# Kernel optimization log

Hardware: AMD Instinct MI355X
Metric: run time of the kernel (lower is better)

Reference implementation:

```python
import jax, jax.numpy as jnp
import numpy as np

B, T, C, H = 4, 2048, 1024, 16
D = C // H  # head dim = 64


def setup_inputs() -> dict:
    key = jax.random.key(0)
    ks = jax.random.split(key, 5)
    s = 1.0 / np.sqrt(C)
    return {
        "x": jax.random.normal(ks[0], (B, T, C), jnp.float32),
        "Wq": jax.random.normal(ks[1], (C, C), jnp.float32) * s,
        "bq": jnp.zeros((C,), jnp.float32),
        "Wk": jax.random.normal(ks[2], (C, C), jnp.float32) * s,
        "bk": jnp.zeros((C,), jnp.float32),
        "Wv": jax.random.normal(ks[3], (C, C), jnp.float32) * s,
        "bv": jnp.zeros((C,), jnp.float32),
        "Wp": jax.random.normal(ks[4], (C, C), jnp.float32) * s,
        "bp": jnp.zeros((C,), jnp.float32),
    }


def reference(x, Wq, bq, Wk, bk, Wv, bv, Wp, bp):
    # linear projections -> [B, H, T, D]
    def heads(t):
        return t.reshape(B, T, H, D).transpose(0, 2, 1, 3)
    q = heads(x @ Wq.T + bq)
    k = heads(x @ Wk.T + bk)
    v = heads(x @ Wv.T + bv)
    scale = 1.0 / np.sqrt(D)
    att = jnp.einsum("bhtd,bhsd->bhts", q, k) * scale  # [B,H,T,T]
    causal = jnp.tril(jnp.ones((T, T), bool))
    att = jnp.where(causal[None, None], att, -jnp.inf)
    att = jax.nn.softmax(att, axis=-1)
    y = jnp.einsum("bhts,bhsd->bhtd", att, v)  # [B,H,T,D]
    y = y.transpose(0, 2, 1, 3).reshape(B, T, C)
    return y @ Wp.T + bp
```

## Files before the change

### kernel.cpp

```cpp
#include <hip/hip_runtime.h>

typedef float f32x4 __attribute__((ext_vector_type(4)));
typedef float f32x16 __attribute__((ext_vector_type(16)));
typedef __bf16 bf16x8 __attribute__((ext_vector_type(8)));
typedef unsigned short u16x8 __attribute__((ext_vector_type(8)));
typedef unsigned int u32x4 __attribute__((ext_vector_type(4)));

#define SCQ 0.1803368801111183f

__device__ inline unsigned short f2bf(float f) {
  unsigned int u = __builtin_bit_cast(unsigned int, f);
  u += 0x7FFFu + ((u >> 16) & 1u);
  return (unsigned short)(u >> 16);
}

__device__ inline float fexp2(float x) {
#if __has_builtin(__builtin_amdgcn_exp2f)
  return __builtin_amdgcn_exp2f(x);
#else
  return exp2f(x);
#endif
}

__device__ inline unsigned int cvtpk_bf16(float a, float b) {
  unsigned int r;
  __asm__("v_cvt_pk_bf16_f32 %0, %1, %2" : "=v"(r) : "v"(a), "v"(b));
  return r;
}
__device__ inline void permswap32(unsigned int& a, unsigned int& b) {
  __asm__("v_permlane32_swap_b32 %0, %1" : "+v"(a), "+v"(b));
}

__device__ inline void gload_lds16(const unsigned short* g, unsigned short* l) {
  __builtin_amdgcn_global_load_lds(
      (const __attribute__((address_space(1))) unsigned int*)g,
      (__attribute__((address_space(3))) unsigned int*)l, 16, 0, 0);
}

__global__ void cvt_x(const float* __restrict__ in, unsigned short* __restrict__ out) {
  int i = (blockIdx.x * 256 + threadIdx.x) * 4;
  float4 f = *(const float4*)(in + i);
  ushort4 o;
  o.x = f2bf(f.x); o.y = f2bf(f.y); o.z = f2bf(f.z); o.w = f2bf(f.w);
  *(ushort4*)(out + i) = o;
}

__global__ void cvt_w(const float* __restrict__ a, const float* __restrict__ b,
                      const float* __restrict__ c, const float* __restrict__ d,
                      unsigned short* __restrict__ oa, unsigned short* __restrict__ ob,
                      unsigned short* __restrict__ oc, unsigned short* __restrict__ od) {
  const float* src[4] = {a, b, c, d};
  unsigned short* dst[4] = {oa, ob, oc, od};
  int m = blockIdx.y;
  int i = (blockIdx.x * 256 + threadIdx.x) * 4;
  float4 f = *(const float4*)(src[m] + i);
  ushort4 o;
  o.x = f2bf(f.x); o.y = f2bf(f.y); o.z = f2bf(f.z); o.w = f2bf(f.w);
  *(ushort4*)(dst[m] + i) = o;
}

template <int MODE>
__global__ __launch_bounds__(512, 2) void gemm8p(const unsigned short* __restrict__ A,
                                                 const unsigned short* __restrict__ Bt,
                                                 const float* __restrict__ b0,
                                                 const float* __restrict__ b1,
                                                 const float* __restrict__ b2,
                                                 void* __restrict__ out,
                                                 int M, int N, int K) {
  __shared__ __align__(16) unsigned short Lg[2][3][128 * 64];
  const int tid = threadIdx.x;
  const int lane = tid & 63, w = tid >> 6;
  const int qm = w >> 2, qn = w & 3;
  const int l15 = lane & 15, kq = lane >> 4;
  const int m0 = blockIdx.x * 128, n0 = blockIdx.y * 256;
  const int NT = K >> 6;

  const int row0 = tid >> 3, c0 = (tid & 7) ^ (row0 & 7);
  const int row1 = row0 + 64, c1 = (tid & 7) ^ (row1 & 7);

  auto stage = [&](int tt, int h) {
    if (tt < NT) {
      const unsigned short* s_ = (h == 0) ? A : Bt;
      const int rbase = (h == 0) ? m0 : (h == 1 ? n0 : n0 + 128);
      unsigned short* d = &Lg[tt & 1][h][0];
      gload_lds16(s_ + (size_t)(rbase + row0) * K + tt * 64 + c0 * 8, d + (size_t)tid * 8);
      gload_lds16(s_ + (size_t)(rbase + row1) * K + tt * 64 + c1 * 8, d + (size_t)(tid + 512) * 8);
    }
  };

  auto rdA = [&](const unsigned short* R, u16x8 (&a)[4][2]) {
#pragma unroll
    for (int mf = 0; mf < 4; mf++) {
      int row = qm * 64 + mf * 16 + l15;
#pragma unroll
      for (int kf = 0; kf < 2; kf++) {
        int pc = (kf * 4 + kq) ^ (row & 7);
        a[mf][kf] = *(const u16x8*)(R + row * 64 + pc * 8);
      }
    }
  };
  auto rdB = [&](const unsigned short* R, u16x8 (&bb)[2][2]) {
#pragma unroll
    for (int nf = 0; nf < 2; nf++) {
      int row = qn * 32 + nf * 16 + l15;
#pragma unroll
      for (int kf = 0; kf < 2; kf++) {
        int pc = (kf * 4 + kq) ^ (row & 7);
        bb[nf][kf] = *(const u16x8*)(R + row * 64 + pc * 8);
      }
    }
  };

  f32x4 acc[4][4] = {};

  auto domfma = [&](u16x8 (&a)[4][2], u16x8 (&bb)[2][2], int hb) {
#pragma unroll
    for (int mf = 0; mf < 4; mf++)
#pragma unroll
      for (int nf = 0; nf < 2; nf++)
#pragma unroll
        for (int kf = 0; kf < 2; kf++)
          acc[mf][hb * 2 + nf] = __builtin_amdgcn_mfma_f32_16x16x32_bf16(
              __builtin_bit_cast(bf16x8, a[mf][kf]),
              __builtin_bit_cast(bf16x8, bb[nf][kf]), acc[mf][hb * 2 + nf], 0, 0, 0);
  };

  stage(0, 0); stage(0, 1); stage(0, 2); stage(1, 0); stage(1, 1);
  __asm__ __volatile__("s_waitcnt vmcnt(4)" ::: "memory");
  __builtin_amdgcn_s_barrier();

  for (int tt = 0; tt < NT; ++tt) {
    const unsigned short* Ar  = &Lg[tt & 1][0][0];
    const unsigned short* B0r = &Lg[tt & 1][1][0];
    const unsigned short* B1r = &Lg[tt & 1][2][0];
    u16x8 aA[4][2], bb[2][2];

    rdA(Ar, aA); rdB(B0r, bb);
    stage(tt + 1, 2);
    __builtin_amdgcn_s_barrier();
    __asm__ __volatile__("s_waitcnt lgkmcnt(0)" ::: "memory");
    __builtin_amdgcn_sched_barrier(0);
    __builtin_amdgcn_s_setprio(1);
    domfma(aA, bb, 0);
    __builtin_amdgcn_s_setprio(0);
    __builtin_amdgcn_s_barrier();

    rdB(B1r, bb);
    stage(tt + 2, 0); stage(tt + 2, 1);
    __builtin_amdgcn_s_barrier();
    __asm__ __volatile__("s_waitcnt lgkmcnt(0)" ::: "memory");
    __builtin_amdgcn_sched_barrier(0);
    __builtin_amdgcn_s_setprio(1);
    domfma(aA, bb, 1);
    __builtin_amdgcn_s_setprio(0);
    if (tt < NT - 2) {
      __asm__ __volatile__("s_waitcnt vmcnt(4)" ::: "memory");
    } else if (tt == NT - 2) {
      __asm__ __volatile__("s_waitcnt vmcnt(0)" ::: "memory");
    }
    __builtin_amdgcn_s_barrier();
  }

#pragma unroll
  for (int nfg = 0; nfg < 4; nfg++) {
    const int col = n0 + (nfg >> 1) * 128 + qn * 32 + (nfg & 1) * 16 + l15;
    float bv, sc;
    int which = 0, cl = col;
    if (MODE == 0) {
      which = col >> 10; cl = col & 1023;
      const float* bp = (which == 0) ? b0 : ((which == 1) ? b1 : b2);
      bv = bp[cl];
      sc = (which == 0) ? SCQ : 1.f;
    } else {
      bv = b0[col]; sc = 1.f;
    }
#pragma unroll
    for (int mf = 0; mf < 4; mf++) {
      f32x4 v4 = acc[mf][nfg];
#pragma unroll
      for (int r = 0; r < 4; r++) {
        int row = m0 + qm * 64 + mf * 16 + kq * 4 + r;
        float v = (v4[r] + bv) * sc;
        if (MODE == 0) {
          int h = cl >> 6, d = cl & 63;
          int b = row >> 11, t = row & 2047;
          ((unsigned short*)out)[(size_t)which * 8388608 +
                                 ((size_t)((b * 16 + h) * 2048 + t)) * 64 + d] = f2bf(v);
        } else {
          ((float*)out)[(size_t)row * N + col] = v;
        }
      }
    }
  }
}

__global__ __launch_bounds__(256) void transpose_v(const unsigned short* __restrict__ V,
                                                   unsigned short* __restrict__ Vt) {
  constexpr int P = 66;
  __shared__ unsigned short L[64 * P];
  const int tid = threadIdx.x;
  const int bh = blockIdx.y;
  const int t0 = blockIdx.x * 64;
  const unsigned short* Vp = V + (size_t)bh * 2048 * 64;
  unsigned short* Op = Vt + (size_t)bh * 64 * 2048;
#pragma unroll
  for (int j = 0; j < 2; j++) {
    int r = (tid >> 3) + j * 32;
    int c = (tid & 7) * 8;
    u16x8 v = *(const u16x8*)(Vp + (size_t)(t0 + r) * 64 + c);
#pragma unroll
    for (int i = 0; i < 4; i++) {
      unsigned int pk = (unsigned int)v[2 * i] | ((unsigned int)v[2 * i + 1] << 16);
      *(unsigned int*)&L[r * P + c + 2 * i] = pk;
    }
  }
  __syncthreads();
#pragma unroll
  for (int j = 0; j < 2; j++) {
    int ch = j * 256 + tid;
    int d = ch >> 3, tc = (ch & 7) * 8;
    u16x8 o;
#pragma unroll
    for (int k = 0; k < 8; k++) o[k] = L[(tc + k) * P + d];
    *(u16x8*)(Op + (size_t)d * 2048 + t0 + tc) = o;
  }
}

__global__ __launch_bounds__(256, 2) void attn_kernel(const unsigned short* __restrict__ Q,
                                                      const unsigned short* __restrict__ Km,
                                                      const unsigned short* __restrict__ Vt,
                                                      unsigned short* __restrict__ Y) {
  constexpr int T = 2048, D = 64;
  __shared__ __align__(16) unsigned short Ks[2][64 * 64];
  __shared__ __align__(16) unsigned short Vs[2][64 * 64];
  const int tid = threadIdx.x;
  const int lane = tid & 63, w = tid >> 6;
  const int l31 = lane & 31, half = lane >> 5;
  const int bh = blockIdx.x;
  const int b = bh >> 4, h = bh & 15;
  const int p = blockIdx.y;
  const unsigned short* Qp = Q + (size_t)bh * T * D;
  const unsigned short* Kp = Km + (size_t)bh * T * D;
  const unsigned short* Vp = Vt + (size_t)bh * D * T;

  const int bch0 = (w * 2) * 64, bch1 = (w * 2 + 1) * 64;
  const int ch0 = bch0 + lane, ch1 = bch1 + lane;
  const int row0 = ch0 >> 3, c0 = (ch0 & 7) ^ (row0 & 7);
  const int row1 = ch1 >> 3, c1 = (ch1 & 7) ^ (row1 & 7);

  for (int phase = 0; phase < 2; ++phase) {
    const int jt = phase ? (63 - (p * 4 + w)) : (p * 4 + w);
    const int qt = jt * 32;
    const int nit = phase ? (32 - 2 * p) : (2 * p + 2);
    const int qg = qt + l31;

    bf16x8 aq[4];
#pragma unroll
    for (int kc = 0; kc < 4; kc++)
      aq[kc] = *(const bf16x8*)(Qp + (size_t)qg * D + kc * 16 + half * 8);
    __asm__ __volatile__("" :: "v"(__builtin_bit_cast(f32x4, aq[0])),
                              "v"(__builtin_bit_cast(f32x4, aq[1])),
                              "v"(__builtin_bit_cast(f32x4, aq[2])),
                              "v"(__builtin_bit_cast(f32x4, aq[3])));

    f32x16 o0 = {}, o1 = {};
    float lsum = 0.f;

    gload_lds16(Kp + (size_t)row0 * 64 + c0 * 8, Ks[0] + bch0 * 8);
    gload_lds16(Kp + (size_t)row1 * 64 + c1 * 8, Ks[0] + bch1 * 8);
    gload_lds16(Vp + (size_t)row0 * T + c0 * 8, Vs[0] + bch0 * 8);
    gload_lds16(Vp + (size_t)row1 * T + c1 * 8, Vs[0] + bch1 * 8);

    int cur = 0;
    for (int it = 0; it < nit; ++it) {
      const int s0 = it * 64;
      if (it + 1 < nit) {
        const int s1 = s0 + 64;
        unsigned short* kd = Ks[cur ^ 1];
        unsigned short* vd = Vs[cur ^ 1];
        gload_lds16(Kp + (size_t)(s1 + row0) * 64 + c0 * 8, kd + bch0 * 8);
        gload_lds16(Kp + (size_t)(s1 + row1) * 64 + c1 * 8, kd + bch1 * 8);
        gload_lds16(Vp + (size_t)row0 * T + s1 + c0 * 8, vd + bch0 * 8);
        gload_lds16(Vp + (size_t)row1 * T + s1 + c1 * 8, vd + bch1 * 8);
        __asm__ __volatile__("s_waitcnt vmcnt(4)" ::: "memory");
      } else {
        __asm__ __volatile__("s_waitcnt vmcnt(0)" ::: "memory");
      }
      __builtin_amdgcn_s_barrier();
      __builtin_amdgcn_sched_barrier(0);

      if (s0 <= qt + 31) {
        const unsigned short* Kb_ = Ks[cur];
        const unsigned short* Vb_ = Vs[cur];

        f32x16 sacc0 = {}, sacc1 = {};
#pragma unroll
        for (int kc = 0; kc < 4; kc++) {
          int kr0 = l31;
          int cc0 = (kc * 2 + half) ^ (kr0 & 7);
          u16x8 k0 = *(const u16x8*)(Kb_ + kr0 * 64 + cc0 * 8);
          sacc0 = __builtin_amdgcn_mfma_f32_32x32x16_bf16(
              __builtin_bit_cast(bf16x8, k0), aq[kc], sacc0, 0, 0, 0);
          int kr1 = 32 + l31;
          int cc1 = (kc * 2 + half) ^ (kr1 & 7);
          u16x8 k1 = *(const u16x8*)(Kb_ + kr1 * 64 + cc1 * 8);
          sacc1 = __builtin_amdgcn_mfma_f32_32x32x16_bf16(
              __builtin_bit_cast(bf16x8, k1), aq[kc], sacc1, 0, 0, 0);
        }

        const bool full = (s0 + 63) <= qt;
        float e0_[16], e1_[16];
        if (full) {
#pragma unroll
          for (int r = 0; r < 16; r++) { e0_[r] = fexp2(sacc0[r]); lsum += e0_[r]; }
#pragma unroll
          for (int r = 0; r < 16; r++) { e1_[r] = fexp2(sacc1[r]); lsum += e1_[r]; }
        } else {
#pragma unroll
          for (int r = 0; r < 16; r++) {
            int sg = s0 + (r & 3) + 8 * (r >> 2) + 4 * half;
            float ex = fexp2(sacc0[r]);
            ex = (sg > qg) ? 0.f : ex;
            e0_[r] = ex; lsum += ex;
          }
#pragma unroll
          for (int r = 0; r < 16; r++) {
            int sg = s0 + 32 + (r & 3) + 8 * (r >> 2) + 4 * half;
            float ex = fexp2(sacc1[r]);
            ex = (sg > qg) ? 0.f : ex;
            e1_[r] = ex; lsum += ex;
          }
        }

        bf16x8 pf[4];
        auto pack2 = [&](const float* e_, int kbase) {
#pragma unroll
          for (int kl = 0; kl < 2; kl++) {
            int base = kl * 8;
            unsigned int a0 = cvtpk_bf16(e_[base + 0], e_[base + 1]);
            unsigned int b0v = cvtpk_bf16(e_[base + 4], e_[base + 5]);
            permswap32(a0, b0v);
            unsigned int a1 = cvtpk_bf16(e_[base + 2], e_[base + 3]);
            unsigned int b1v = cvtpk_bf16(e_[base + 6], e_[base + 7]);
            permswap32(a1, b1v);
            u32x4 t = {a0, a1, b0v, b1v};
            pf[kbase + kl] = __builtin_bit_cast(bf16x8, t);
          }
        };
        pack2(e0_, 0);
        pack2(e1_, 2);

#pragma unroll
        for (int kc = 0; kc < 4; kc++) {
          int vr0 = l31;
          int cc0 = (kc * 2 + half) ^ (vr0 & 7);
          u16x8 v0 = *(const u16x8*)(Vb_ + vr0 * 64 + cc0 * 8);
          o0 = __builtin_amdgcn_mfma_f32_32x32x16_bf16(
              __builtin_bit_cast(bf16x8, v0), pf[kc], o0, 0, 0, 0);
          int vr1 = 32 + l31;
          int cc1 = (kc * 2 + half) ^ (vr1 & 7);
          u16x8 v1 = *(const u16x8*)(Vb_ + vr1 * 64 + cc1 * 8);
          o1 = __builtin_amdgcn_mfma_f32_32x32x16_bf16(
              __builtin_bit_cast(bf16x8, v1), pf[kc], o1, 0, 0, 0);
        }
      }

      __builtin_amdgcn_sched_barrier(0);
      __builtin_amdgcn_s_barrier();
      cur ^= 1;
    }

    float tot = lsum + __shfl_xor(lsum, 32);
    float inv = 1.f / tot;
    unsigned short* Yrow = Y + ((size_t)(b * T + qg)) * 1024 + h * 64;
#pragma unroll
    for (int rp = 0; rp < 8; rp++) {
      int r = rp * 2;
      int d = (r & 3) + 8 * (r >> 2) + 4 * half;
      *(unsigned int*)(Yrow + d)      = cvtpk_bf16(o0[r] * inv, o0[r + 1] * inv);
      *(unsigned int*)(Yrow + 32 + d) = cvtpk_bf16(o1[r] * inv, o1[r + 1] * inv);
    }
  }
}

extern "C" void kernel_launch(void* const* d_in, const int* in_sizes, int n_in,
                              void* d_out, int out_size, void* d_ws, size_t ws_size,
                              hipStream_t stream) {
  const float* x  = (const float*)d_in[0];
  const float* Wq = (const float*)d_in[1];
  const float* bq = (const float*)d_in[2];
  const float* Wk = (const float*)d_in[3];
  const float* bk = (const float*)d_in[4];
  const float* Wv = (const float*)d_in[5];
  const float* bv = (const float*)d_in[6];
  const float* Wp = (const float*)d_in[7];
  const float* bp = (const float*)d_in[8];

  char* ws = (char*)d_ws;
  unsigned short* xb  = (unsigned short*)(ws + 0);
  unsigned short* wqb = (unsigned short*)(ws + 16777216);
  unsigned short* wkb = (unsigned short*)(ws + 18874368);
  unsigned short* wvb = (unsigned short*)(ws + 20971520);
  unsigned short* wpb = (unsigned short*)(ws + 23068672);
  unsigned short* Qb  = (unsigned short*)(ws + 25165824);
  unsigned short* Kb  = (unsigned short*)(ws + 41943040);
  unsigned short* Vb  = (unsigned short*)(ws + 58720256);
  unsigned short* Vtb = xb;
  unsigned short* Yb  = Vb;

  cvt_x<<<8192, 256, 0, stream>>>(x, xb);
  cvt_w<<<dim3(1024, 4), 256, 0, stream>>>(Wq, Wk, Wv, Wp, wqb, wkb, wvb, wpb);

  gemm8p<0><<<dim3(64, 12), 512, 0, stream>>>(xb, wqb, bq, bk, bv, Qb, 8192, 3072, 1024);

  transpose_v<<<dim3(32, 64), 256, 0, stream>>>(Vb, Vtb);
  attn_kernel<<<dim3(64, 8), 256, 0, stream>>>(Qb, Kb, Vtb, Yb);

  gemm8p<1><<<dim3(64, 4), 512, 0, stream>>>(Yb, wpb, bp, bp, bp, d_out, 8192, 1024, 1024);
}
```

Before: 248.5 us.

## Fuse V transpose into QKV GEMM epilogue and merge conversion kernels

Replaces the tuned 8-wave pipelined QKV GEMM with a simpler 128x128 tile GEMM using 32x32 MFMA. For the V columns, the epilogue transposes through LDS and writes Vt directly, which removes the separate transpose kernel and one round trip of V through memory. The two fp32-to-bf16 conversion kernels are merged into a single launch. The trade-off is that the new GEMM has no double buffering or prefetch overlap, so the QKV projection itself may run slower than the pipelined kernel it replaces.

```diff
diff --git a/kernel.cpp b/kernel.cpp
--- a/kernel.cpp
+++ b/kernel.cpp
@@ -37,26 +37,143 @@
       (__attribute__((address_space(3))) unsigned int*)l, 16, 0, 0);
 }
 
-__global__ void cvt_x(const float* __restrict__ in, unsigned short* __restrict__ out) {
-  int i = (blockIdx.x * 256 + threadIdx.x) * 4;
-  float4 f = *(const float4*)(in + i);
+__global__ void cvt_all(const float* __restrict__ x,
+                        const float* __restrict__ wq, const float* __restrict__ wk,
+                        const float* __restrict__ wv, const float* __restrict__ wp,
+                        unsigned short* __restrict__ xb,
+                        unsigned short* __restrict__ oq, unsigned short* __restrict__ ok,
+                        unsigned short* __restrict__ ov, unsigned short* __restrict__ op_) {
+  int gid = blockIdx.x;
+  const float* src;
+  unsigned short* dst;
+  int i;
+  if (gid < 8192) {
+    src = x; dst = xb;
+    i = (gid * 256 + threadIdx.x) * 4;
+  } else {
+    int g = gid - 8192;
+    int m = g >> 10;
+    src = (m == 0) ? wq : (m == 1) ? wk : (m == 2) ? wv : wp;
+    dst = (m == 0) ? oq : (m == 1) ? ok : (m == 2) ? ov : op_;
+    i = ((g & 1023) * 256 + threadIdx.x) * 4;
+  }
+  float4 f = *(const float4*)(src + i);
   ushort4 o;
   o.x = f2bf(f.x); o.y = f2bf(f.y); o.z = f2bf(f.z); o.w = f2bf(f.w);
-  *(ushort4*)(out + i) = o;
-}
-
-__global__ void cvt_w(const float* __restrict__ a, const float* __restrict__ b,
-                      const float* __restrict__ c, const float* __restrict__ d,
-                      unsigned short* __restrict__ oa, unsigned short* __restrict__ ob,
-                      unsigned short* __restrict__ oc, unsigned short* __restrict__ od) {
-  const float* src[4] = {a, b, c, d};
-  unsigned short* dst[4] = {oa, ob, oc, od};
-  int m = blockIdx.y;
-  int i = (blockIdx.x * 256 + threadIdx.x) * 4;
-  float4 f = *(const float4*)(src[m] + i);
-  ushort4 o;
-  o.x = f2bf(f.x); o.y = f2bf(f.y); o.z = f2bf(f.z); o.w = f2bf(f.w);
-  *(ushort4*)(dst[m] + i) = o;
+  *(ushort4*)(dst + i) = o;
+}
+
+template <int MODE>
+__global__ __launch_bounds__(256) void gemm128(const unsigned short* __restrict__ A,
+                                               const unsigned short* __restrict__ Bt,
+                                               const float* __restrict__ b0,
+                                               const float* __restrict__ b1,
+                                               const float* __restrict__ b2,
+                                               void* __restrict__ out,
+                                               unsigned short* __restrict__ vt,
+                                               int M, int N, int K) {
+  __shared__ __align__(16) unsigned short Sh[2][128 * 64];
+  unsigned short* As = Sh[0];
+  unsigned short* Bs = Sh[1];
+  const int tid = threadIdx.x;
+  const int lane = tid & 63, w = tid >> 6;
+  const int l31 = lane & 31, half = lane >> 5;
+  const int wm = w & 1, wn = w >> 1;
+  const int m0 = blockIdx.x * 128, n0 = blockIdx.y * 128;
+
+  f32x16 acc[2][2] = {};
+
+  for (int kb = 0; kb < K; kb += 64) {
+#pragma unroll
+    for (int j = 0; j < 4; j++) {
+      int ch = j * 256 + w * 64 + lane;
+      int row = ch >> 3, pc = ch & 7;
+      int c = pc ^ (row & 7);
+      gload_lds16(A + (size_t)(m0 + row) * K + kb + c * 8, As + (size_t)(j * 256 + w * 64) * 8);
+      gload_lds16(Bt + (size_t)(n0 + row) * K + kb + c * 8, Bs + (size_t)(j * 256 + w * 64) * 8);
+    }
+    __syncthreads();
+#pragma unroll
+    for (int ks = 0; ks < 64; ks += 16) {
+      bf16x8 af[2], bfr[2];
+#pragma unroll
+      for (int at = 0; at < 2; at++) {
+        int row = wm * 64 + at * 32 + l31;
+        int pc = ((ks >> 3) + half) ^ (row & 7);
+        af[at] = *(const bf16x8*)(As + row * 64 + pc * 8);
+      }
+#pragma unroll
+      for (int nt = 0; nt < 2; nt++) {
+        int row = wn * 64 + nt * 32 + l31;
+        int pc = ((ks >> 3) + half) ^ (row & 7);
+        bfr[nt] = *(const bf16x8*)(Bs + row * 64 + pc * 8);
+      }
+#pragma unroll
+      for (int at = 0; at < 2; at++)
+#pragma unroll
+        for (int nt = 0; nt < 2; nt++)
+          acc[at][nt] = __builtin_amdgcn_mfma_f32_32x32x16_bf16(af[at], bfr[nt], acc[at][nt], 0, 0, 0);
+    }
+    __syncthreads();
+  }
+
+  if (MODE == 0 && n0 >= 2048) {
+    unsigned short* Lt = &Sh[0][0];
+#pragma unroll
+    for (int at = 0; at < 2; at++)
+#pragma unroll
+      for (int nt = 0; nt < 2; nt++) {
+        int d = wn * 64 + nt * 32 + l31;
+        float bv = b2[(n0 & 1023) + d];
+        int swz = (d & 31) << 2;
+#pragma unroll
+        for (int reg = 0; reg < 16; reg++) {
+          int t = wm * 64 + at * 32 + (reg & 3) + 8 * (reg >> 2) + 4 * half;
+          Lt[d * 128 + (t ^ swz)] = f2bf(acc[at][nt][reg] + bv);
+        }
+      }
+    __syncthreads();
+    const int bb = m0 >> 11, t0 = m0 & 2047;
+#pragma unroll
+    for (int i = 0; i < 16; i++) {
+      int d = (tid >> 5) + i * 8;
+      int tb = (tid & 31) * 4;
+      ushort4 val = *(const ushort4*)&Lt[d * 128 + (tb ^ ((d & 31) << 2))];
+      int h = ((n0 & 1023) + d) >> 6;
+      *(ushort4*)(vt + ((size_t)((bb * 16 + h) * 64 + (d & 63))) * 2048 + t0 + tb) = val;
+    }
+    return;
+  }
+
+#pragma unroll
+  for (int at = 0; at < 2; at++)
+#pragma unroll
+    for (int nt = 0; nt < 2; nt++) {
+      int col = n0 + wn * 64 + nt * 32 + l31;
+      float bv, sc;
+      int which = 0, cl = col;
+      if (MODE == 0) {
+        which = col >> 10; cl = col & 1023;
+        const float* bp = (which == 0) ? b0 : b1;
+        bv = bp[cl];
+        sc = (which == 0) ? SCQ : 1.f;
+      } else {
+        bv = b0[col]; sc = 1.f;
+      }
+#pragma unroll
+      for (int reg = 0; reg < 16; reg++) {
+        int row = m0 + wm * 64 + at * 32 + (reg & 3) + 8 * (reg >> 2) + 4 * half;
+        float v = (acc[at][nt][reg] + bv) * sc;
+        if (MODE == 0) {
+          int h = cl >> 6, d = cl & 63;
+          int b = row >> 11, t = row & 2047;
+          ((unsigned short*)out)[(size_t)which * 8388608 +
+                                 ((size_t)((b * 16 + h) * 2048 + t)) * 64 + d] = f2bf(v);
+        } else {
+          ((float*)out)[(size_t)row * N + col] = v;
+        }
+      }
+    }
 }
 
 template <int MODE>
@@ -164,65 +281,16 @@
 #pragma unroll
   for (int nfg = 0; nfg < 4; nfg++) {
     const int col = n0 + (nfg >> 1) * 128 + qn * 32 + (nfg & 1) * 16 + l15;
-    float bv, sc;
-    int which = 0, cl = col;
-    if (MODE == 0) {
-      which = col >> 10; cl = col & 1023;
-      const float* bp = (which == 0) ? b0 : ((which == 1) ? b1 : b2);
-      bv = bp[cl];
-      sc = (which == 0) ? SCQ : 1.f;
-    } else {
-      bv = b0[col]; sc = 1.f;
-    }
+    float bv = b0[col];
 #pragma unroll
     for (int mf = 0; mf < 4; mf++) {
       f32x4 v4 = acc[mf][nfg];
 #pragma unroll
       for (int r = 0; r < 4; r++) {
         int row = m0 + qm * 64 + mf * 16 + kq * 4 + r;
-        float v = (v4[r] + bv) * sc;
-        if (MODE == 0) {
-          int h = cl >> 6, d = cl & 63;
-          int b = row >> 11, t = row & 2047;
-          ((unsigned short*)out)[(size_t)which * 8388608 +
-                                 ((size_t)((b * 16 + h) * 2048 + t)) * 64 + d] = f2bf(v);
-        } else {
-          ((float*)out)[(size_t)row * N + col] = v;
-        }
-      }
-    }
-  }
-}
-
-__global__ __launch_bounds__(256) void transpose_v(const unsigned short* __restrict__ V,
-                                                   unsigned short* __restrict__ Vt) {
-  constexpr int P = 66;
-  __shared__ unsigned short L[64 * P];
-  const int tid = threadIdx.x;
-  const int bh = blockIdx.y;
-  const int t0 = blockIdx.x * 64;
-  const unsigned short* Vp = V + (size_t)bh * 2048 * 64;
-  unsigned short* Op = Vt + (size_t)bh * 64 * 2048;
-#pragma unroll
-  for (int j = 0; j < 2; j++) {
-    int r = (tid >> 3) + j * 32;
-    int c = (tid & 7) * 8;
-    u16x8 v = *(const u16x8*)(Vp + (size_t)(t0 + r) * 64 + c);
-#pragma unroll
-    for (int i = 0; i < 4; i++) {
-      unsigned int pk = (unsigned int)v[2 * i] | ((unsigned int)v[2 * i + 1] << 16);
-      *(unsigned int*)&L[r * P + c + 2 * i] = pk;
-    }
-  }
-  __syncthreads();
-#pragma unroll
-  for (int j = 0; j < 2; j++) {
-    int ch = j * 256 + tid;
-    int d = ch >> 3, tc = (ch & 7) * 8;
-    u16x8 o;
-#pragma unroll
-    for (int k = 0; k < 8; k++) o[k] = L[(tc + k) * P + d];
-    *(u16x8*)(Op + (size_t)d * 2048 + t0 + tc) = o;
+        ((float*)out)[(size_t)row * N + col] = v4[r] + bv;
+      }
+    }
   }
 }
 
@@ -404,16 +472,13 @@
   unsigned short* wpb = (unsigned short*)(ws + 23068672);
   unsigned short* Qb  = (unsigned short*)(ws + 25165824);
   unsigned short* Kb  = (unsigned short*)(ws + 41943040);
-  unsigned short* Vb  = (unsigned short*)(ws + 58720256);
-  unsigned short* Vtb = xb;
-  unsigned short* Yb  = Vb;
-
-  cvt_x<<<8192, 256, 0, stream>>>(x, xb);
-  cvt_w<<<dim3(1024, 4), 256, 0, stream>>>(Wq, Wk, Wv, Wp, wqb, wkb, wvb, wpb);
-
-  gemm8p<0><<<dim3(64, 12), 512, 0, stream>>>(xb, wqb, bq, bk, bv, Qb, 8192, 3072, 1024);
-
-  transpose_v<<<dim3(32, 64), 256, 0, stream>>>(Vb, Vtb);
+  unsigned short* Vtb = (unsigned short*)(ws + 58720256);
+  unsigned short* Yb  = xb;
+
+  cvt_all<<<12288, 256, 0, stream>>>(x, Wq, Wk, Wv, Wp, xb, wqb, wkb, wvb, wpb);
+
+  gemm128<0><<<dim3(64, 24), 256, 0, stream>>>(xb, wqb, bq, bk, bv, Qb, Vtb, 8192, 3072, 1024);
+
   attn_kernel<<<dim3(64, 8), 256, 0, stream>>>(Qb, Kb, Vtb, Yb);
 
   gemm8p<1><<<dim3(64, 4), 512, 0, stream>>>(Yb, wpb, bp, bp, bp, d_out, 8192, 1024, 1024);
```

After: 236.8 us. 1.05x faster.
